# Kernel tuning notes

Measured on AMD Instinct MI355X. Metric: run time of the kernel, lower is better.

Reference implementation:

```python
import jax, jax.numpy as jnp
import numpy as np
import math

D_MODEL = 512
H = 8
DK = D_MODEL // H  # 64
B, S = 2, 4096


def setup_inputs() -> dict:
    key = jax.random.key(0)
    ks = jax.random.split(key, 11)
    sc = 1.0 / math.sqrt(D_MODEL)
    return {
        "query": jax.random.normal(ks[0], (B, S, D_MODEL), jnp.float32),
        "key": jax.random.normal(ks[1], (B, S, D_MODEL), jnp.float32),
        "value": jax.random.normal(ks[2], (B, S, D_MODEL), jnp.float32),
        "Wq": jax.random.normal(ks[3], (D_MODEL, D_MODEL), jnp.float32) * sc,
        "bq": jnp.zeros((D_MODEL,), jnp.float32),
        "Wk": jax.random.normal(ks[4], (D_MODEL, D_MODEL), jnp.float32) * sc,
        "bk": jnp.zeros((D_MODEL,), jnp.float32),
        "Wv": jax.random.normal(ks[5], (D_MODEL, D_MODEL), jnp.float32) * sc,
        "bv": jnp.zeros((D_MODEL,), jnp.float32),
        "Wo": jax.random.normal(ks[6], (D_MODEL, D_MODEL), jnp.float32) * sc,
        "bo": jnp.zeros((D_MODEL,), jnp.float32),
    }


def reference(query, key, value, Wq, bq, Wk, bk, Wv, bv, Wo, bo):
    b = query.shape[0]
    # projections; W stored [in, out]
    def proj(x, W, bias):
        y = x @ W + bias                      # [B,S,h*dk]
        return y.reshape(b, -1, H, DK).transpose(0, 2, 1, 3)  # [B,h,S,dk]

    q = proj(query, Wq, bq)
    k = proj(key, Wk, bk)
    v = proj(value, Wv, bv)
    scores = jnp.einsum("bhqd,bhkd->bhqk", q, k) / math.sqrt(DK)
    attn = jax.nn.softmax(scores, axis=-1)    # [B,h,Sq,Sk]
    ctx = jnp.einsum("bhqk,bhkd->bhqd", attn, v)
    ctx = ctx.transpose(0, 2, 1, 3).reshape(b, -1, H * DK)  # [B,S,d_model]
    return ctx @ Wo + bo
```

## Files before the change

### kernel.cpp

```cpp
#include <hip/hip_runtime.h>
#include <hip/hip_bf16.h>

#define DM   512
#define HEADS 8
#define DKH  64
#define BATCH 2
#define SEQ  4096

typedef float  f32x4  __attribute__((ext_vector_type(4)));
typedef __bf16 bf16x8 __attribute__((ext_vector_type(8)));
typedef __bf16 bf16x4 __attribute__((ext_vector_type(4)));

static __device__ __forceinline__ f32x4 mfma16(bf16x8 a, bf16x8 b, f32x4 c) {
    return __builtin_amdgcn_mfma_f32_16x16x32_bf16(a, b, c, 0, 0, 0);
}

__global__ __launch_bounds__(256) void wt_convert(const float* __restrict__ W,
                                                  __bf16* __restrict__ Wt) {
    __shared__ float tile[32][33];
    const int tx = threadIdx.x & 31, ty = threadIdx.x >> 5;
    const int nb = blockIdx.x * 32, kb = blockIdx.y * 32;
#pragma unroll
    for (int i = 0; i < 4; ++i)
        tile[ty + 8 * i][tx] = W[(size_t)(kb + ty + 8 * i) * DM + nb + tx];
    __syncthreads();
#pragma unroll
    for (int i = 0; i < 4; ++i)
        Wt[(size_t)(nb + ty + 8 * i) * DM + kb + tx] = (__bf16)tile[tx][ty + 8 * i];
}

struct Ptr3 { const void* A; const __bf16* Bt; const float* bias; void* Out; };
struct GemmArgs { Ptr3 p[3]; };

template <bool A_FP32, bool OUT_BF16>
__global__ __launch_bounds__(256) void gemm_tile(GemmArgs args) {
    __shared__ __bf16 Al[128][72];
    __shared__ __bf16 Bl[128][72];
    const Ptr3 P = args.p[blockIdx.z];
    const int tid = threadIdx.x;
    const int lane = tid & 63, wid = tid >> 6;
    const int lq = lane & 15, hi = lane >> 4;
    const int m0 = blockIdx.x * 128, n0 = blockIdx.y * 128;
    const int wm = (wid >> 1) * 64, wn = (wid & 1) * 64;

    f32x4 acc[4][4] = {};

    for (int kt = 0; kt < DM / 64; ++kt) {
        const int k0 = kt * 64;
        bf16x8 abuf[4], bbuf[4];
        if (A_FP32) {
            const float* A = (const float*)P.A;
#pragma unroll
            for (int i = 0; i < 4; ++i) {
                int c = tid + 256 * i, row = c >> 3, cc = c & 7;
                const f32x4* src = (const f32x4*)&A[(size_t)(m0 + row) * DM + k0 + cc * 8];
                f32x4 f0 = src[0], f1 = src[1];
                bf16x8 v;
                v[0] = (__bf16)f0[0]; v[1] = (__bf16)f0[1]; v[2] = (__bf16)f0[2]; v[3] = (__bf16)f0[3];
                v[4] = (__bf16)f1[0]; v[5] = (__bf16)f1[1]; v[6] = (__bf16)f1[2]; v[7] = (__bf16)f1[3];
                abuf[i] = v;
            }
        } else {
            const __bf16* A = (const __bf16*)P.A;
#pragma unroll
            for (int i = 0; i < 4; ++i) {
                int c = tid + 256 * i, row = c >> 3, cc = c & 7;
                abuf[i] = *(const bf16x8*)&A[(size_t)(m0 + row) * DM + k0 + cc * 8];
            }
        }
        {
            const __bf16* Bt = P.Bt;
#pragma unroll
            for (int i = 0; i < 4; ++i) {
                int c = tid + 256 * i, row = c >> 3, cc = c & 7;
                bbuf[i] = *(const bf16x8*)&Bt[(size_t)(n0 + row) * DM + k0 + cc * 8];
            }
        }
        if (kt) __syncthreads();
#pragma unroll
        for (int i = 0; i < 4; ++i) {
            int c = tid + 256 * i, row = c >> 3, cc = c & 7;
            *(bf16x8*)&Al[row][cc * 8] = abuf[i];
            *(bf16x8*)&Bl[row][cc * 8] = bbuf[i];
        }
        __syncthreads();
#pragma unroll
        for (int ks = 0; ks < 2; ++ks) {
            bf16x8 af[4], bfv[4];
#pragma unroll
            for (int i = 0; i < 4; ++i)
                af[i] = *(const bf16x8*)&Al[wm + i * 16 + lq][ks * 32 + hi * 8];
#pragma unroll
            for (int j = 0; j < 4; ++j)
                bfv[j] = *(const bf16x8*)&Bl[wn + j * 16 + lq][ks * 32 + hi * 8];
#pragma unroll
            for (int i = 0; i < 4; ++i)
#pragma unroll
                for (int j = 0; j < 4; ++j)
                    acc[i][j] = mfma16(af[i], bfv[j], acc[i][j]);
        }
    }
    const float* bias = P.bias;
#pragma unroll
    for (int j = 0; j < 4; ++j) {
        const int n = n0 + wn + j * 16 + lq;
        const float bv = bias[n];
#pragma unroll
        for (int i = 0; i < 4; ++i) {
#pragma unroll
            for (int r = 0; r < 4; ++r) {
                const int m = m0 + wm + i * 16 + hi * 4 + r;
                const float v = acc[i][j][r] + bv;
                if (OUT_BF16) ((__bf16*)P.Out)[(size_t)m * DM + n] = (__bf16)v;
                else          ((float*)P.Out)[(size_t)m * DM + n] = v;
            }
        }
    }
}

__global__ __launch_bounds__(256) void v_transpose(const __bf16* __restrict__ Vp,
                                                   __bf16* __restrict__ Vt) {
    __shared__ __bf16 tile[64][72];
    const int tid = threadIdx.x;
    const int tt = blockIdx.x * 64;
    const int bh = blockIdx.y, b = bh >> 3, h = bh & 7;
#pragma unroll
    for (int i = 0; i < 2; ++i) {
        int c = tid + 256 * i, row = c >> 3, cc = c & 7;
        *(bf16x8*)&tile[row][cc * 8] =
            *(const bf16x8*)&Vp[(size_t)(b * SEQ + tt + row) * DM + h * DKH + cc * 8];
    }
    __syncthreads();
#pragma unroll
    for (int i = 0; i < 2; ++i) {
        int c = tid + 256 * i, row = c >> 3, cc = c & 7;
        bf16x8 v;
#pragma unroll
        for (int j = 0; j < 8; ++j) v[j] = tile[cc * 8 + j][row];
        *(bf16x8*)&Vt[(size_t)(bh * DKH + row) * SEQ + tt + cc * 8] = v;
    }
}

__global__ __launch_bounds__(256) void flash_attn(const __bf16* __restrict__ Qp,
                                                  const __bf16* __restrict__ Kp,
                                                  const __bf16* __restrict__ Vt,
                                                  __bf16* __restrict__ Ctx) {
    __shared__ __bf16 Kl[64][72];
    __shared__ __bf16 Vl[64][72];
    __shared__ __bf16 Pl[4][16][72];
    const int tid = threadIdx.x;
    const int lane = tid & 63, w = tid >> 6;
    const int lq = lane & 15, hi = lane >> 4;
    const int qt = blockIdx.x, bh = blockIdx.y, b = bh >> 3, h = bh & 7;
    const int qrow = qt * 64 + w * 16 + lq;

    bf16x8 qf[2];
#pragma unroll
    for (int ks = 0; ks < 2; ++ks)
        qf[ks] = *(const bf16x8*)&Qp[(size_t)(b * SEQ + qrow) * DM + h * DKH + ks * 32 + hi * 8];

    f32x4 acc[4] = {};
    float m_run = -__builtin_inff(), l_run = 0.f;

    for (int kvt = 0; kvt < SEQ / 64; ++kvt) {
        const int kv0 = kvt * 64;
        bf16x8 kbuf[2], vbuf[2];
#pragma unroll
        for (int i = 0; i < 2; ++i) {
            int c = tid + 256 * i, row = c >> 3, cc = c & 7;
            kbuf[i] = *(const bf16x8*)&Kp[(size_t)(b * SEQ + kv0 + row) * DM + h * DKH + cc * 8];
            vbuf[i] = *(const bf16x8*)&Vt[(size_t)(bh * DKH + row) * SEQ + kv0 + cc * 8];
        }
        if (kvt) __syncthreads();
#pragma unroll
        for (int i = 0; i < 2; ++i) {
            int c = tid + 256 * i, row = c >> 3, cc = c & 7;
            *(bf16x8*)&Kl[row][cc * 8] = kbuf[i];
            *(bf16x8*)&Vl[row][cc * 8] = vbuf[i];
        }
        __syncthreads();

        f32x4 s[4] = {};
#pragma unroll
        for (int ks = 0; ks < 2; ++ks) {
#pragma unroll
            for (int mt = 0; mt < 4; ++mt) {
                bf16x8 kf = *(const bf16x8*)&Kl[mt * 16 + lq][ks * 32 + hi * 8];
                s[mt] = mfma16(kf, qf[ks], s[mt]);
            }
        }

        float mx = m_run;
        float sc[4][4];
#pragma unroll
        for (int mt = 0; mt < 4; ++mt)
#pragma unroll
            for (int r = 0; r < 4; ++r) {
                float v = s[mt][r] * 0.125f;
                sc[mt][r] = v;
                mx = fmaxf(mx, v);
            }
        mx = fmaxf(mx, __shfl_xor(mx, 16));
        mx = fmaxf(mx, __shfl_xor(mx, 32));
        const float alpha = __expf(m_run - mx);
        m_run = mx;
        float lsum = 0.f;
#pragma unroll
        for (int mt = 0; mt < 4; ++mt) {
            bf16x4 pb;
#pragma unroll
            for (int r = 0; r < 4; ++r) {
                float p = __expf(sc[mt][r] - mx);
                lsum += p;
                pb[r] = (__bf16)p;
            }
            *(bf16x4*)&Pl[w][lq][mt * 16 + hi * 4] = pb;
        }
        lsum += __shfl_xor(lsum, 16);
        lsum += __shfl_xor(lsum, 32);
        l_run = l_run * alpha + lsum;

        float ar[4];
#pragma unroll
        for (int r = 0; r < 4; ++r) ar[r] = __shfl(alpha, hi * 4 + r);
#pragma unroll
        for (int nt = 0; nt < 4; ++nt)
#pragma unroll
            for (int r = 0; r < 4; ++r) acc[nt][r] *= ar[r];

#pragma unroll
        for (int ks = 0; ks < 2; ++ks) {
            bf16x8 pf = *(const bf16x8*)&Pl[w][lq][ks * 32 + hi * 8];
#pragma unroll
            for (int nt = 0; nt < 4; ++nt) {
                bf16x8 vf = *(const bf16x8*)&Vl[nt * 16 + lq][ks * 32 + hi * 8];
                acc[nt] = mfma16(pf, vf, acc[nt]);
            }
        }
    }

    float lr[4];
#pragma unroll
    for (int r = 0; r < 4; ++r) lr[r] = __shfl(l_run, hi * 4 + r);
#pragma unroll
    for (int nt = 0; nt < 4; ++nt)
#pragma unroll
        for (int r = 0; r < 4; ++r) {
            const int m = qt * 64 + w * 16 + hi * 4 + r;
            const float o = acc[nt][r] / lr[r];
            Ctx[(size_t)(b * SEQ + m) * DM + h * DKH + nt * 16 + lq] = (__bf16)o;
        }
}

extern "C" void kernel_launch(void* const* d_in, const int* in_sizes, int n_in,
                              void* d_out, int out_size, void* d_ws, size_t ws_size,
                              hipStream_t stream) {
    (void)in_sizes; (void)n_in; (void)out_size;
    const float* query = (const float*)d_in[0];
    const float* key_  = (const float*)d_in[1];
    const float* value = (const float*)d_in[2];
    const float* Wq = (const float*)d_in[3];
    const float* bq = (const float*)d_in[4];
    const float* Wk = (const float*)d_in[5];
    const float* bk = (const float*)d_in[6];
    const float* Wv = (const float*)d_in[7];
    const float* bv = (const float*)d_in[8];
    const float* Wo = (const float*)d_in[9];
    const float* bo = (const float*)d_in[10];

    char* ws = (char*)d_ws;
    const size_t WSZ = (size_t)512 * 1024;
    const size_t XSZ = (size_t)8 * 1024 * 1024;
    if (ws_size < 4 * WSZ + 5 * XSZ) return;
    __bf16* Wtq = (__bf16*)(ws);
    __bf16* Wtk = (__bf16*)(ws + WSZ);
    __bf16* Wtv = (__bf16*)(ws + 2 * WSZ);
    __bf16* Wto = (__bf16*)(ws + 3 * WSZ);
    char* xb = ws + 4 * WSZ;
    __bf16* Qp  = (__bf16*)(xb);
    __bf16* Kp  = (__bf16*)(xb + XSZ);
    __bf16* Vp  = (__bf16*)(xb + 2 * XSZ);
    __bf16* Vt  = (__bf16*)(xb + 3 * XSZ);
    __bf16* Ctx = (__bf16*)(xb + 4 * XSZ);

    wt_convert<<<dim3(16, 16), 256, 0, stream>>>(Wq, Wtq);
    wt_convert<<<dim3(16, 16), 256, 0, stream>>>(Wk, Wtk);
    wt_convert<<<dim3(16, 16), 256, 0, stream>>>(Wv, Wtv);
    wt_convert<<<dim3(16, 16), 256, 0, stream>>>(Wo, Wto);

    GemmArgs qa;
    qa.p[0] = {query, Wtq, bq, Qp};
    qa.p[1] = {key_,  Wtk, bk, Kp};
    qa.p[2] = {value, Wtv, bv, Vp};
    gemm_tile<true, true><<<dim3(64, 4, 3), 256, 0, stream>>>(qa);

    v_transpose<<<dim3(SEQ / 64, BATCH * HEADS), 256, 0, stream>>>(Vp, Vt);

    flash_attn<<<dim3(SEQ / 64, BATCH * HEADS), 256, 0, stream>>>(Qp, Kp, Vt, Ctx);

    GemmArgs oa;
    oa.p[0] = {Ctx, Wto, bo, d_out};
    oa.p[1] = oa.p[0]; oa.p[2] = oa.p[0];
    gemm_tile<false, false><<<dim3(64, 4, 1), 256, 0, stream>>>(oa);
}
```

Before: 304.6 us.

## Rewrite flash attention with 32x32 MFMA, async LDS double buffering and lazy rescale

Replaces the attention kernel with one in which each wave handles 32 query rows using 32x32x16 bf16 MFMA. K/V tiles are loaded directly into swizzled LDS via global_load_lds with double buffering. The softmax scale and log2e are folded into the Q projection so the kernel can use exp2, and P is kept in registers via lane shuffles instead of a round trip through LDS. It also adds a lazy max rescale with a threshold of 8, priority hints around the MFMAs, and merges the four weight-convert launches into one. The lazy rescale lets unnormalized values grow before they are rescaled, and the new layout and swizzle logic is more complex to get right.

```diff
diff --git a/kernel.cpp b/kernel.cpp
--- a/kernel.cpp
+++ b/kernel.cpp
@@ -8,15 +8,27 @@
 #define SEQ  4096
 
 typedef float  f32x4  __attribute__((ext_vector_type(4)));
+typedef float  f32x16 __attribute__((ext_vector_type(16)));
 typedef __bf16 bf16x8 __attribute__((ext_vector_type(8)));
 typedef __bf16 bf16x4 __attribute__((ext_vector_type(4)));
+typedef __bf16 bf16x2 __attribute__((ext_vector_type(2)));
 
 static __device__ __forceinline__ f32x4 mfma16(bf16x8 a, bf16x8 b, f32x4 c) {
     return __builtin_amdgcn_mfma_f32_16x16x32_bf16(a, b, c, 0, 0, 0);
 }
-
-__global__ __launch_bounds__(256) void wt_convert(const float* __restrict__ W,
-                                                  __bf16* __restrict__ Wt) {
+static __device__ __forceinline__ f32x16 mfma32(bf16x8 a, bf16x8 b, f32x16 c) {
+    return __builtin_amdgcn_mfma_f32_32x32x16_bf16(a, b, c, 0, 0, 0);
+}
+
+#define GLD16(gp, lp) __builtin_amdgcn_global_load_lds( \
+    (const __attribute__((address_space(1))) void*)(gp), \
+    (__attribute__((address_space(3))) void*)(lp), 16, 0, 0)
+
+struct WtAll { const float* W[4]; __bf16* Wt[4]; };
+
+__global__ __launch_bounds__(256) void wt_convert_all(WtAll a) {
+    const float* W = a.W[blockIdx.z];
+    __bf16* Wt = a.Wt[blockIdx.z];
     __shared__ float tile[32][33];
     const int tx = threadIdx.x & 31, ty = threadIdx.x >> 5;
     const int nb = blockIdx.x * 32, kb = blockIdx.y * 32;
@@ -29,7 +41,7 @@
         Wt[(size_t)(nb + ty + 8 * i) * DM + kb + tx] = (__bf16)tile[tx][ty + 8 * i];
 }
 
-struct Ptr3 { const void* A; const __bf16* Bt; const float* bias; void* Out; };
+struct Ptr3 { const void* A; const __bf16* Bt; const float* bias; void* Out; float ascale; };
 struct GemmArgs { Ptr3 p[3]; };
 
 template <bool A_FP32, bool OUT_BF16>
@@ -101,6 +113,7 @@
         }
     }
     const float* bias = P.bias;
+    const float asc = P.ascale;
 #pragma unroll
     for (int j = 0; j < 4; ++j) {
         const int n = n0 + wn + j * 16 + lq;
@@ -110,7 +123,7 @@
 #pragma unroll
             for (int r = 0; r < 4; ++r) {
                 const int m = m0 + wm + i * 16 + hi * 4 + r;
-                const float v = acc[i][j][r] + bv;
+                const float v = (acc[i][j][r] + bv) * asc;
                 if (OUT_BF16) ((__bf16*)P.Out)[(size_t)m * DM + n] = (__bf16)v;
                 else          ((float*)P.Out)[(size_t)m * DM + n] = v;
             }
@@ -141,115 +154,148 @@
     }
 }
 
-__global__ __launch_bounds__(256) void flash_attn(const __bf16* __restrict__ Qp,
-                                                  const __bf16* __restrict__ Kp,
-                                                  const __bf16* __restrict__ Vt,
-                                                  __bf16* __restrict__ Ctx) {
-    __shared__ __bf16 Kl[64][72];
-    __shared__ __bf16 Vl[64][72];
-    __shared__ __bf16 Pl[4][16][72];
-    const int tid = threadIdx.x;
-    const int lane = tid & 63, w = tid >> 6;
-    const int lq = lane & 15, hi = lane >> 4;
-    const int qt = blockIdx.x, bh = blockIdx.y, b = bh >> 3, h = bh & 7;
-    const int qrow = qt * 64 + w * 16 + lq;
-
-    bf16x8 qf[2];
-#pragma unroll
-    for (int ks = 0; ks < 2; ++ks)
-        qf[ks] = *(const bf16x8*)&Qp[(size_t)(b * SEQ + qrow) * DM + h * DKH + ks * 32 + hi * 8];
-
-    f32x4 acc[4] = {};
+__global__ __launch_bounds__(256) void flash_attn2(const __bf16* __restrict__ Qp,
+                                                   const __bf16* __restrict__ Kp,
+                                                   const __bf16* __restrict__ Vt,
+                                                   __bf16* __restrict__ Ctx) {
+    __shared__ __bf16 Kl[2][64][64];
+    __shared__ __bf16 Vl[2][64][64];
+    __shared__ float  Lbuf[4][32];
+
+    const int tid = threadIdx.x, lane = tid & 63, w = tid >> 6;
+    const int c = lane & 31, h = lane >> 5;
+    const int bh = blockIdx.y, b = bh >> 3, hd = bh & 7;
+    const int qbase = blockIdx.x * 128 + w * 32;
+
+    bf16x8 qf[4];
+#pragma unroll
+    for (int t = 0; t < 4; ++t)
+        qf[t] = *(const bf16x8*)&Qp[(size_t)(b * SEQ + qbase + c) * DM + hd * DKH + 16 * t + 8 * h];
+
+    const int r0 = w * 16 + (lane >> 3);
+    const int r1 = r0 + 8;
+    const int s0 = (lane & 7) ^ ((r0 ^ (r0 >> 3)) & 7);
+    const int s1 = (lane & 7) ^ ((r1 ^ (r1 >> 3)) & 7);
+    const __bf16* kg0 = Kp + (size_t)(b * SEQ + r0) * DM + hd * DKH + s0 * 8;
+    const __bf16* kg1 = Kp + (size_t)(b * SEQ + r1) * DM + hd * DKH + s1 * 8;
+    const __bf16* vg0 = Vt + (size_t)(bh * DKH + r0) * SEQ + s0 * 8;
+    const __bf16* vg1 = Vt + (size_t)(bh * DKH + r1) * SEQ + s1 * 8;
+
+    const int swz0 = (c ^ (c >> 3)) & 7;
+    const int swz1 = ((32 + c) ^ ((32 + c) >> 3)) & 7;
+    const int rowb0 = c * 128, rowb1 = (32 + c) * 128;
+    const char* kb = (const char*)&Kl[0][0][0];
+    const char* vb = (const char*)&Vl[0][0][0];
+
+    f32x16 acc0 = {}, acc1 = {};
     float m_run = -__builtin_inff(), l_run = 0.f;
 
-    for (int kvt = 0; kvt < SEQ / 64; ++kvt) {
-        const int kv0 = kvt * 64;
-        bf16x8 kbuf[2], vbuf[2];
-#pragma unroll
-        for (int i = 0; i < 2; ++i) {
-            int c = tid + 256 * i, row = c >> 3, cc = c & 7;
-            kbuf[i] = *(const bf16x8*)&Kp[(size_t)(b * SEQ + kv0 + row) * DM + h * DKH + cc * 8];
-            vbuf[i] = *(const bf16x8*)&Vt[(size_t)(bh * DKH + row) * SEQ + kv0 + cc * 8];
-        }
-        if (kvt) __syncthreads();
-#pragma unroll
-        for (int i = 0; i < 2; ++i) {
-            int c = tid + 256 * i, row = c >> 3, cc = c & 7;
-            *(bf16x8*)&Kl[row][cc * 8] = kbuf[i];
-            *(bf16x8*)&Vl[row][cc * 8] = vbuf[i];
-        }
+    GLD16(kg0, &Kl[0][w * 16][0]);
+    GLD16(kg1, &Kl[0][w * 16 + 8][0]);
+    GLD16(vg0, &Vl[0][w * 16][0]);
+    GLD16(vg1, &Vl[0][w * 16 + 8][0]);
+    __syncthreads();
+
+    const int NT = SEQ / 64;
+    for (int kvt = 0; kvt < NT; ++kvt) {
+        const int cur = kvt & 1;
+        if (kvt + 1 < NT) {
+            const size_t ko = (size_t)(kvt + 1) * 64 * DM;
+            const size_t vo = (size_t)(kvt + 1) * 64;
+            GLD16(kg0 + ko, &Kl[cur ^ 1][w * 16][0]);
+            GLD16(kg1 + ko, &Kl[cur ^ 1][w * 16 + 8][0]);
+            GLD16(vg0 + vo, &Vl[cur ^ 1][w * 16][0]);
+            GLD16(vg1 + vo, &Vl[cur ^ 1][w * 16 + 8][0]);
+        }
+        const char* kc = kb + cur * (64 * 128);
+        const char* vc = vb + cur * (64 * 128);
+
+        f32x16 sa = {}, sb = {};
+        __builtin_amdgcn_s_setprio(1);
+#pragma unroll
+        for (int t = 0; t < 4; ++t) {
+            bf16x8 kf0 = *(const bf16x8*)(kc + rowb0 + (((2 * t + h) ^ swz0) << 4));
+            sa = mfma32(kf0, qf[t], sa);
+            bf16x8 kf1 = *(const bf16x8*)(kc + rowb1 + (((2 * t + h) ^ swz1) << 4));
+            sb = mfma32(kf1, qf[t], sb);
+        }
+        __builtin_amdgcn_s_setprio(0);
+
+        float mx = sa[0];
+#pragma unroll
+        for (int r = 1; r < 16; ++r) mx = fmaxf(mx, sa[r]);
+#pragma unroll
+        for (int r = 0; r < 16; ++r) mx = fmaxf(mx, sb[r]);
+        mx = fmaxf(mx, __shfl_xor(mx, 32));
+        if (!__all(mx <= m_run + 8.f)) {
+            const float mnew = fmaxf(m_run, mx);
+            const float al = __builtin_amdgcn_exp2f(m_run - mnew);
+            m_run = mnew;
+            l_run *= al;
+            if (lane < 32) Lbuf[w][lane] = al;
+#pragma unroll
+            for (int r = 0; r < 16; ++r) {
+                const float a2 = Lbuf[w][(r & 3) + 8 * (r >> 2) + 4 * h];
+                acc0[r] *= a2; acc1[r] *= a2;
+            }
+        }
+        float ls = 0.f;
+        float pa[16], pb[16];
+#pragma unroll
+        for (int r = 0; r < 16; ++r) { pa[r] = __builtin_amdgcn_exp2f(sa[r] - m_run); ls += pa[r]; }
+#pragma unroll
+        for (int r = 0; r < 16; ++r) { pb[r] = __builtin_amdgcn_exp2f(sb[r] - m_run); ls += pb[r]; }
+        ls += __shfl_xor(ls, 32);
+        l_run += ls;
+
+        int ua[4][2], ub[4][2];
+#pragma unroll
+        for (int q4 = 0; q4 < 4; ++q4)
+#pragma unroll
+            for (int i = 0; i < 2; ++i) {
+                bf16x2 ta; ta[0] = (__bf16)pa[4 * q4 + 2 * i]; ta[1] = (__bf16)pa[4 * q4 + 2 * i + 1];
+                ua[q4][i] = __builtin_bit_cast(int, ta);
+                bf16x2 tb; tb[0] = (__bf16)pb[4 * q4 + 2 * i]; tb[1] = (__bf16)pb[4 * q4 + 2 * i + 1];
+                ub[q4][i] = __builtin_bit_cast(int, tb);
+            }
+
+#define EXCH(U, tl, W0, W1, W2, W3) do {                         \
+            int z0 = h ? (U)[2*(tl)][0] : (U)[2*(tl)+1][0];      \
+            int y0 = __shfl_xor(z0, 32);                         \
+            W0 = h ? y0 : (U)[2*(tl)][0];                        \
+            W2 = h ? (U)[2*(tl)+1][0] : y0;                      \
+            int z1 = h ? (U)[2*(tl)][1] : (U)[2*(tl)+1][1];      \
+            int y1 = __shfl_xor(z1, 32);                         \
+            W1 = h ? y1 : (U)[2*(tl)][1];                        \
+            W3 = h ? (U)[2*(tl)+1][1] : y1; } while (0)
+
+#pragma unroll
+        for (int tg = 0; tg < 4; ++tg) {
+            int w0, w1, w2, w3;
+            if (tg < 2) { EXCH(ua, tg, w0, w1, w2, w3); }
+            else        { EXCH(ub, (tg - 2), w0, w1, w2, w3); }
+            union { int i4[4]; bf16x8 v; } pf;
+            pf.i4[0] = w0; pf.i4[1] = w1; pf.i4[2] = w2; pf.i4[3] = w3;
+            bf16x8 vf0 = *(const bf16x8*)(vc + rowb0 + (((2 * tg + h) ^ swz0) << 4));
+            bf16x8 vf1 = *(const bf16x8*)(vc + rowb1 + (((2 * tg + h) ^ swz1) << 4));
+            __builtin_amdgcn_s_setprio(1);
+            acc0 = mfma32(pf.v, vf0, acc0);
+            acc1 = mfma32(pf.v, vf1, acc1);
+            __builtin_amdgcn_s_setprio(0);
+        }
+#undef EXCH
         __syncthreads();
-
-        f32x4 s[4] = {};
-#pragma unroll
-        for (int ks = 0; ks < 2; ++ks) {
-#pragma unroll
-            for (int mt = 0; mt < 4; ++mt) {
-                bf16x8 kf = *(const bf16x8*)&Kl[mt * 16 + lq][ks * 32 + hi * 8];
-                s[mt] = mfma16(kf, qf[ks], s[mt]);
-            }
-        }
-
-        float mx = m_run;
-        float sc[4][4];
-#pragma unroll
-        for (int mt = 0; mt < 4; ++mt)
-#pragma unroll
-            for (int r = 0; r < 4; ++r) {
-                float v = s[mt][r] * 0.125f;
-                sc[mt][r] = v;
-                mx = fmaxf(mx, v);
-            }
-        mx = fmaxf(mx, __shfl_xor(mx, 16));
-        mx = fmaxf(mx, __shfl_xor(mx, 32));
-        const float alpha = __expf(m_run - mx);
-        m_run = mx;
-        float lsum = 0.f;
-#pragma unroll
-        for (int mt = 0; mt < 4; ++mt) {
-            bf16x4 pb;
-#pragma unroll
-            for (int r = 0; r < 4; ++r) {
-                float p = __expf(sc[mt][r] - mx);
-                lsum += p;
-                pb[r] = (__bf16)p;
-            }
-            *(bf16x4*)&Pl[w][lq][mt * 16 + hi * 4] = pb;
-        }
-        lsum += __shfl_xor(lsum, 16);
-        lsum += __shfl_xor(lsum, 32);
-        l_run = l_run * alpha + lsum;
-
-        float ar[4];
-#pragma unroll
-        for (int r = 0; r < 4; ++r) ar[r] = __shfl(alpha, hi * 4 + r);
-#pragma unroll
-        for (int nt = 0; nt < 4; ++nt)
-#pragma unroll
-            for (int r = 0; r < 4; ++r) acc[nt][r] *= ar[r];
-
-#pragma unroll
-        for (int ks = 0; ks < 2; ++ks) {
-            bf16x8 pf = *(const bf16x8*)&Pl[w][lq][ks * 32 + hi * 8];
-#pragma unroll
-            for (int nt = 0; nt < 4; ++nt) {
-                bf16x8 vf = *(const bf16x8*)&Vl[nt * 16 + lq][ks * 32 + hi * 8];
-                acc[nt] = mfma16(pf, vf, acc[nt]);
-            }
-        }
-    }
-
-    float lr[4];
-#pragma unroll
-    for (int r = 0; r < 4; ++r) lr[r] = __shfl(l_run, hi * 4 + r);
-#pragma unroll
-    for (int nt = 0; nt < 4; ++nt)
-#pragma unroll
-        for (int r = 0; r < 4; ++r) {
-            const int m = qt * 64 + w * 16 + hi * 4 + r;
-            const float o = acc[nt][r] / lr[r];
-            Ctx[(size_t)(b * SEQ + m) * DM + h * DKH + nt * 16 + lq] = (__bf16)o;
-        }
+    }
+
+    if (lane < 32) Lbuf[w][lane] = l_run;
+    __bf16* outp = Ctx + (size_t)(b * SEQ + qbase) * DM + hd * DKH;
+#pragma unroll
+    for (int r = 0; r < 16; ++r) {
+        const int qr = (r & 3) + 8 * (r >> 2) + 4 * h;
+        const float li = 1.f / Lbuf[w][qr];
+        outp[(size_t)qr * DM + c]      = (__bf16)(acc0[r] * li);
+        outp[(size_t)qr * DM + 32 + c] = (__bf16)(acc1[r] * li);
+    }
 }
 
 extern "C" void kernel_launch(void* const* d_in, const int* in_sizes, int n_in,
@@ -283,23 +329,24 @@
     __bf16* Vt  = (__bf16*)(xb + 3 * XSZ);
     __bf16* Ctx = (__bf16*)(xb + 4 * XSZ);
 
-    wt_convert<<<dim3(16, 16), 256, 0, stream>>>(Wq, Wtq);
-    wt_convert<<<dim3(16, 16), 256, 0, stream>>>(Wk, Wtk);
-    wt_convert<<<dim3(16, 16), 256, 0, stream>>>(Wv, Wtv);
-    wt_convert<<<dim3(16, 16), 256, 0, stream>>>(Wo, Wto);
-
+    WtAll wa;
+    wa.W[0] = Wq; wa.W[1] = Wk; wa.W[2] = Wv; wa.W[3] = Wo;
+    wa.Wt[0] = Wtq; wa.Wt[1] = Wtk; wa.Wt[2] = Wtv; wa.Wt[3] = Wto;
+    wt_convert_all<<<dim3(16, 16, 4), 256, 0, stream>>>(wa);
+
+    const float QSC = 0.125f * 1.4426950408889634f;
     GemmArgs qa;
-    qa.p[0] = {query, Wtq, bq, Qp};
-    qa.p[1] = {key_,  Wtk, bk, Kp};
-    qa.p[2] = {value, Wtv, bv, Vp};
+    qa.p[0] = {query, Wtq, bq, Qp, QSC};
+    qa.p[1] = {key_,  Wtk, bk, Kp, 1.0f};
+    qa.p[2] = {value, Wtv, bv, Vp, 1.0f};
     gemm_tile<true, true><<<dim3(64, 4, 3), 256, 0, stream>>>(qa);
 
     v_transpose<<<dim3(SEQ / 64, BATCH * HEADS), 256, 0, stream>>>(Vp, Vt);
 
-    flash_attn<<<dim3(SEQ / 64, BATCH * HEADS), 256, 0, stream>>>(Qp, Kp, Vt, Ctx);
+    flash_attn2<<<dim3(SEQ / 128, BATCH * HEADS), 256, 0, stream>>>(Qp, Kp, Vt, Ctx);
 
     GemmArgs oa;
-    oa.p[0] = {Ctx, Wto, bo, d_out};
+    oa.p[0] = {Ctx, Wto, bo, d_out, 1.0f};
     oa.p[1] = oa.p[0]; oa.p[2] = oa.p[0];
     gemm_tile<false, false><<<dim3(64, 4, 1), 256, 0, stream>>>(oa);
 }
```

Result: faster. 255.5 us (-16.1%).
